# Performance work log

Measured on AMD Instinct MI355X. Metric: run time of the kernel, lower is better.

The kernel has to match this reference:

```python
import jax, jax.numpy as jnp
import numpy as np

NEG_SLOPE = 0.2


def gat_layer(x, src, dst, W, att_src, att_dst, bias, heads, ch, n):
    # x: [N, Din]; W: [Din, heads*ch]
    xl = (x @ W).reshape(n, heads, ch)                # [N, H, C]
    a_s = jnp.sum(xl * att_src[None], axis=-1)        # [N, H]
    a_d = jnp.sum(xl * att_dst[None], axis=-1)        # [N, H]
    e = jax.nn.leaky_relu(a_s[src] + a_d[dst], NEG_SLOPE)   # [E, H]
    # segment softmax over incoming edges per destination node
    emax = jax.ops.segment_max(e, dst, num_segments=n)      # [N, H]
    ex = jnp.exp(e - emax[dst])
    denom = jax.ops.segment_sum(ex, dst, num_segments=n)
    alpha = ex / denom[dst]                                  # [E, H]
    msg = xl[src] * alpha[:, :, None]                        # [E, H, C]
    out = jax.ops.segment_sum(msg, dst, num_segments=n)      # [N, H, C]
    return out.reshape(n, heads * ch) + bias


def setup_inputs() -> dict:
    key = jax.random.key(0)
    ks = jax.random.split(key, 10)
    N, D, H, C, E, NCLS = 10000, 128, 4, 256, 160000, 10
    s = 0.05
    return {
        "x": jax.random.normal(ks[0], (N, D), jnp.float32),
        "edge_index": jax.random.randint(ks[1], (2, E), 0, N, jnp.int64),
        "W1": jax.random.normal(ks[2], (D, H * C), jnp.float32) * s,
        "att_src1": jax.random.normal(ks[3], (H, C), jnp.float32) * s,
        "att_dst1": jax.random.normal(ks[4], (H, C), jnp.float32) * s,
        "b1": jnp.zeros((H * C,), jnp.float32),
        "W2": jax.random.normal(ks[5], (H * C, C), jnp.float32) * s,
        "att_src2": jax.random.normal(ks[6], (1, C), jnp.float32) * s,
        "att_dst2": jax.random.normal(ks[7], (1, C), jnp.float32) * s,
        "b2": jnp.zeros((C,), jnp.float32),
        "Wc": jax.random.normal(ks[8], (C, NCLS), jnp.float32) * s,
        "bc": jnp.zeros((NCLS,), jnp.float32),
    }


def reference(x, edge_index, W1, att_src1, att_dst1, b1, W2, att_src2, att_dst2, b2, Wc, bc):
    n = x.shape[0]
    # PyG GATConv adds self-loops by default
    loops = jnp.arange(n, dtype=edge_index.dtype)
    src = jnp.concatenate([edge_index[0], loops])
    dst = jnp.concatenate([edge_index[1], loops])
    h1 = jax.nn.relu(gat_layer(x, src, dst, W1, att_src1, att_dst1, b1, 4, 256, n))
    h2 = jax.nn.relu(gat_layer(h1, src, dst, W2, att_src2, att_dst2, b2, 1, 256, n))
    z = jnp.mean(h2, axis=0, keepdims=True)[None]   # global_mean_pool (single graph), unsqueeze(0) -> [1,1,C]
    return z @ Wc + bc                               # [1,1,n_cls]
```

## Files before the change

### kernel.cpp

```cpp
#include <hip/hip_runtime.h>
#include <hip/hip_bf16.h>
#include <math.h>

#define NEG_SLOPE 0.2f

typedef __attribute__((ext_vector_type(8))) short short8;
typedef __attribute__((ext_vector_type(4))) float f32x4;

typedef __attribute__((address_space(1))) const void g_void;
typedef __attribute__((address_space(3))) void l_void;

__device__ __forceinline__ float lrelu(float x) { return x > 0.f ? x : NEG_SLOPE * x; }
__device__ __forceinline__ float bf2f(unsigned short u) { return __uint_as_float((unsigned)u << 16); }
__device__ __forceinline__ unsigned short f2bf(float f) {
    unsigned u = __float_as_uint(f);
    unsigned rounding = 0x7fff + ((u >> 16) & 1);
    return (unsigned short)((u + rounding) >> 16);
}

__device__ __forceinline__ void transpose_part(const float* __restrict__ in,
                                               unsigned short* __restrict__ out,
                                               int R, int Cc, int bx, int by,
                                               int tx, int ty)
{
    __shared__ float tile[32][33];
    int c0 = bx * 32, r0 = by * 32;
#pragma unroll
    for (int j = 0; j < 4; ++j)
        tile[ty + j * 8][tx] = in[(size_t)(r0 + ty + j * 8) * Cc + c0 + tx];
    __syncthreads();
#pragma unroll
    for (int j = 0; j < 4; ++j)
        out[(size_t)(c0 + ty + j * 8) * R + r0 + tx] = f2bf(tile[tx][ty + j * 8]);
}

__global__ __launch_bounds__(256) void prep(const float* __restrict__ x,
                                            unsigned short* __restrict__ x_bf,
                                            const float* __restrict__ W1,
                                            unsigned short* __restrict__ w1t,
                                            const float* __restrict__ W2,
                                            unsigned short* __restrict__ w2t,
                                            int n_valid4, int nb_conv)
{
    const int bid = blockIdx.x;
    const int tid = threadIdx.x;
    if (bid < nb_conv) {
        int g = bid * 256 + tid;
        ushort4 o;
        if (g < n_valid4) {
            float4 v = *reinterpret_cast<const float4*>(x + (size_t)g * 4);
            o = make_ushort4(f2bf(v.x), f2bf(v.y), f2bf(v.z), f2bf(v.w));
        } else {
            o = make_ushort4(0, 0, 0, 0);
        }
        *reinterpret_cast<ushort4*>(x_bf + (size_t)g * 4) = o;
    } else if (bid < nb_conv + 128) {
        int b = bid - nb_conv;
        transpose_part(W1, w1t, 128, 1024, b & 31, b >> 5, tid & 31, tid >> 5);
    } else {
        int b = bid - nb_conv - 128;
        transpose_part(W2, w2t, 1024, 256, b & 7, b >> 3, tid & 31, tid >> 5);
    }
}

__global__ __launch_bounds__(256) void watt_k(const unsigned short* __restrict__ w1t,
                                              const float* __restrict__ as1,
                                              const float* __restrict__ ad1,
                                              float* __restrict__ watt)
{
    const int b = blockIdx.x;
    const int h = b >> 1, sd = b & 1;
    const float* att = (sd ? ad1 : as1) + h * 256;
    const int k = threadIdx.x & 127;
    const int chalf = threadIdx.x >> 7;
    float s = 0.f;
#pragma unroll 8
    for (int c = chalf * 128; c < chalf * 128 + 128; ++c)
        s = fmaf(bf2f(w1t[(size_t)(h * 256 + c) * 128 + k]), att[c], s);
    __shared__ float sh[256];
    sh[threadIdx.x] = s;
    __syncthreads();
    if (chalf == 0) watt[sd * 512 + h * 128 + k] = s + sh[128 + k];
}

__global__ __launch_bounds__(256) void score1(const unsigned short* __restrict__ x_bf,
                                              const float* __restrict__ watt,
                                              float* __restrict__ a_s,
                                              float* __restrict__ a_d, int N)
{
    const int n = blockIdx.x * 4 + (threadIdx.x >> 6);
    const int lane = threadIdx.x & 63;
    if (n >= N) return;
    unsigned u = *reinterpret_cast<const unsigned*>(x_bf + (size_t)n * 128 + lane * 2);
    float x0 = bf2f((unsigned short)(u & 0xffff)), x1 = bf2f((unsigned short)(u >> 16));
    float s[4], d[4];
#pragma unroll
    for (int h = 0; h < 4; ++h) {
        float2 ws = *reinterpret_cast<const float2*>(watt + h * 128 + lane * 2);
        float2 wd = *reinterpret_cast<const float2*>(watt + 512 + h * 128 + lane * 2);
        s[h] = x0 * ws.x + x1 * ws.y;
        d[h] = x0 * wd.x + x1 * wd.y;
    }
#pragma unroll
    for (int o = 32; o > 0; o >>= 1) {
#pragma unroll
        for (int h = 0; h < 4; ++h) {
            s[h] += __shfl_xor(s[h], o);
            d[h] += __shfl_xor(d[h], o);
        }
    }
    if (lane == 0) {
        *reinterpret_cast<float4*>(a_s + (size_t)n * 4) = make_float4(s[0], s[1], s[2], s[3]);
        *reinterpret_cast<float4*>(a_d + (size_t)n * 4) = make_float4(d[0], d[1], d[2], d[3]);
    }
}

__global__ __launch_bounds__(256) void gemm_bf16(const unsigned short* __restrict__ A, int lda,
                                                 size_t strideAz,
                                                 const unsigned short* __restrict__ Bt, int ldb,
                                                 size_t strideBz,
                                                 unsigned short* __restrict__ C, int ldc, int colz,
                                                 const float* __restrict__ bias, int relu,
                                                 int K)
{
    __shared__ unsigned short sA[128 * 64];
    __shared__ unsigned short sB[128 * 64];
    const int zb = blockIdx.z;
    A += (size_t)zb * strideAz;
    Bt += (size_t)zb * strideBz;
    const int ccol0 = zb * colz;
    const int tid = threadIdx.x;
    const int lane = tid & 63;
    const int w = tid >> 6;
    const int wr = w >> 1, wc = w & 1;
    const int m0 = blockIdx.y * 128;
    const int n0 = blockIdx.x * 128;

    f32x4 acc[4][4];
#pragma unroll
    for (int i = 0; i < 4; ++i)
#pragma unroll
        for (int j = 0; j < 4; ++j) acc[i][j] = (f32x4){0.f, 0.f, 0.f, 0.f};

    const int lrow = lane >> 3;
    const int lchunk = (lane & 7) ^ lrow;

    for (int k0 = 0; k0 < K; k0 += 64) {
#pragma unroll
        for (int i = 0; i < 4; ++i) {
            int r0 = (w * 4 + i) * 8;
            const unsigned short* g = A + (size_t)(m0 + r0 + lrow) * lda + k0 + lchunk * 8;
            __builtin_amdgcn_global_load_lds((g_void*)g, (l_void*)((char*)sA + r0 * 128), 16, 0, 0);
        }
#pragma unroll
        for (int i = 0; i < 4; ++i) {
            int r0 = (w * 4 + i) * 8;
            const unsigned short* g = Bt + (size_t)(n0 + r0 + lrow) * ldb + k0 + lchunk * 8;
            __builtin_amdgcn_global_load_lds((g_void*)g, (l_void*)((char*)sB + r0 * 128), 16, 0, 0);
        }
        __syncthreads();
#pragma unroll
        for (int kk = 0; kk < 2; ++kk) {
            short8 a[4], b[4];
#pragma unroll
            for (int i = 0; i < 4; ++i) {
                int r = wr * 64 + i * 16 + (lane & 15);
                int sw = (kk * 4 + (lane >> 4)) ^ (r & 7);
                a[i] = *reinterpret_cast<const short8*>(&sA[r * 64 + sw * 8]);
            }
#pragma unroll
            for (int j = 0; j < 4; ++j) {
                int r = wc * 64 + j * 16 + (lane & 15);
                int sw = (kk * 4 + (lane >> 4)) ^ (r & 7);
                b[j] = *reinterpret_cast<const short8*>(&sB[r * 64 + sw * 8]);
            }
#pragma unroll
            for (int i = 0; i < 4; ++i)
#pragma unroll
                for (int j = 0; j < 4; ++j)
                    acc[i][j] = __builtin_amdgcn_mfma_f32_16x16x32_bf16(a[i], b[j], acc[i][j], 0, 0, 0);
        }
        __syncthreads();
    }

#pragma unroll
    for (int i = 0; i < 4; ++i) {
        int row_b = m0 + wr * 64 + i * 16 + (lane >> 4) * 4;
#pragma unroll
        for (int j = 0; j < 4; ++j) {
            int col = n0 + wc * 64 + j * 16 + (lane & 15);
            float bv = bias ? bias[ccol0 + col] : 0.f;
#pragma unroll
            for (int r = 0; r < 4; ++r) {
                float v = acc[i][j][r] + bv;
                if (relu) v = fmaxf(v, 0.f);
                C[(size_t)(row_b + r) * ldc + ccol0 + col] = f2bf(v);
            }
        }
    }
}

__global__ __launch_bounds__(256) void attn_scores(const unsigned short* __restrict__ xl,
                                                   const float* __restrict__ att_s,
                                                   const float* __restrict__ att_d,
                                                   float* __restrict__ a_s,
                                                   float* __restrict__ a_d,
                                                   int NH, int H)
{
    int wid = (blockIdx.x * 256 + threadIdx.x) >> 6;
    int lane = threadIdx.x & 63;
    if (wid >= NH) return;
    int h = wid % H;
    ushort4 v = *reinterpret_cast<const ushort4*>(xl + (size_t)wid * 256 + lane * 4);
    float4 vs = *reinterpret_cast<const float4*>(att_s + h * 256 + lane * 4);
    float4 vd = *reinterpret_cast<const float4*>(att_d + h * 256 + lane * 4);
    float x0 = bf2f(v.x), x1 = bf2f(v.y), x2 = bf2f(v.z), x3 = bf2f(v.w);
    float ss = x0 * vs.x + x1 * vs.y + x2 * vs.z + x3 * vs.w;
    float sd = x0 * vd.x + x1 * vd.y + x2 * vd.z + x3 * vd.w;
#pragma unroll
    for (int o = 32; o > 0; o >>= 1) {
        ss += __shfl_down(ss, o);
        sd += __shfl_down(sd, o);
    }
    if (lane == 0) { a_s[wid] = ss; a_d[wid] = sd; }
}

__global__ __launch_bounds__(256) void count_deg(const int* __restrict__ ei, int E, int E2,
                                                 int* __restrict__ counts)
{
    int e = blockIdx.x * 256 + threadIdx.x;
    if (e >= E2) return;
    int dd = (e < E) ? ei[E + e] : (e - E);
    atomicAdd(&counts[dd], 1);
}

__global__ __launch_bounds__(256) void scan1(const int* __restrict__ counts,
                                             int* __restrict__ offs,
                                             int* __restrict__ btot, int n)
{
    int b = blockIdx.x, tid = threadIdx.x, i = b * 256 + tid;
    int lane = tid & 63, w = tid >> 6;
    int v = (i < n) ? counts[i] : 0;
    int s = v;
#pragma unroll
    for (int o = 1; o < 64; o <<= 1) {
        int t = __shfl_up(s, o);
        if (lane >= o) s += t;
    }
    __shared__ int wsum[4];
    if (lane == 63) wsum[w] = s;
    __syncthreads();
    int base = 0;
#pragma unroll
    for (int k = 0; k < 4; ++k)
        if (k < w) base += wsum[k];
    int incl = s + base;
    if (i < n) offs[i] = incl - v;
    if (tid == 255) btot[b] = incl;
}

__global__ __launch_bounds__(256) void scan2(int* __restrict__ offs,
                                             const int* __restrict__ btot, int n)
{
    int b = blockIdx.x, tid = threadIdx.x, i = b * 256 + tid;
    __shared__ int sbase;
    if (tid < 64) {
        int v = (tid < b) ? btot[tid] : 0;
#pragma unroll
        for (int o = 32; o > 0; o >>= 1) v += __shfl_down(v, o);
        if (tid == 0) sbase = v;
    }
    __syncthreads();
    if (i < n) offs[i] += sbase;
    if (b == (int)gridDim.x - 1 && tid == 255) offs[n] = sbase + btot[b];
}

__global__ __launch_bounds__(256) void scatter_csr(const int* __restrict__ ei, int E, int E2,
                                                   const int* __restrict__ offsets,
                                                   int* __restrict__ cursor,
                                                   int* __restrict__ csr_src)
{
    int e = blockIdx.x * 256 + threadIdx.x;
    if (e >= E2) return;
    int s, dd;
    if (e < E) { s = ei[e]; dd = ei[E + e]; }
    else       { s = e - E; dd = e - E; }
    int pos = offsets[dd] + atomicAdd(&cursor[dd], 1);
    csr_src[pos] = s;
}

__global__ __launch_bounds__(64) void alpha_h4(const float* __restrict__ a_s,
                                               const float* __restrict__ a_d,
                                               const int* __restrict__ offsets,
                                               const int* __restrict__ csr_src,
                                               float* __restrict__ alpha)
{
    const int dst = blockIdx.x;
    const int lane = threadIdx.x;
    const int o0 = offsets[dst];
    const int deg = offsets[dst + 1] - o0;
    const int h = lane & 3;
    const int i0 = lane >> 2;
    const float adh = a_d[dst * 4 + h];

    float m = -1e30f;
    for (int i = i0; i < deg; i += 16)
        m = fmaxf(m, lrelu(a_s[csr_src[o0 + i] * 4 + h] + adh));
#pragma unroll
    for (int o = 4; o < 64; o <<= 1) m = fmaxf(m, __shfl_xor(m, o));
    float sum = 0.f;
    for (int i = i0; i < deg; i += 16)
        sum += __expf(lrelu(a_s[csr_src[o0 + i] * 4 + h] + adh) - m);
#pragma unroll
    for (int o = 4; o < 64; o <<= 1) sum += __shfl_xor(sum, o);
    const float inv = 1.f / sum;
    for (int i = i0; i < deg; i += 16)
        alpha[(size_t)(o0 + i) * 4 + h] =
            __expf(lrelu(a_s[csr_src[o0 + i] * 4 + h] + adh) - m) * inv;
}

__global__ __launch_bounds__(64) void alpha_h1(const float* __restrict__ a_s,
                                               const float* __restrict__ a_d,
                                               const int* __restrict__ offsets,
                                               const int* __restrict__ csr_src,
                                               float* __restrict__ alpha)
{
    const int dst = blockIdx.x;
    const int lane = threadIdx.x;
    const int o0 = offsets[dst];
    const int deg = offsets[dst + 1] - o0;
    const float ad = a_d[dst];

    float m = -1e30f;
    for (int i = lane; i < deg; i += 64)
        m = fmaxf(m, lrelu(a_s[csr_src[o0 + i]] + ad));
#pragma unroll
    for (int o = 1; o < 64; o <<= 1) m = fmaxf(m, __shfl_xor(m, o));
    float sum = 0.f;
    for (int i = lane; i < deg; i += 64)
        sum += __expf(lrelu(a_s[csr_src[o0 + i]] + ad) - m);
#pragma unroll
    for (int o = 1; o < 64; o <<= 1) sum += __shfl_xor(sum, o);
    const float inv = 1.f / sum;
    for (int i = lane; i < deg; i += 64)
        alpha[o0 + i] = __expf(lrelu(a_s[csr_src[o0 + i]] + ad) - m) * inv;
}

__global__ __launch_bounds__(256) void zgather(const unsigned short* __restrict__ x_bf,
                                               const float* __restrict__ alpha,
                                               const int* __restrict__ offs,
                                               const int* __restrict__ csr,
                                               unsigned short* __restrict__ z,
                                               int N, int Mpad)
{
    const int wid = threadIdx.x >> 6, lane = threadIdx.x & 63;
    const int dst = blockIdx.x * 4 + wid;
    if (dst >= Mpad) return;
    const size_t zoff = (size_t)dst * 128 + lane * 2;
    if (dst >= N) {
#pragma unroll
        for (int h = 0; h < 4; ++h)
            *reinterpret_cast<unsigned*>(z + (size_t)h * Mpad * 128 + zoff) = 0u;
        return;
    }
    const int o0 = offs[dst];
    const int deg = offs[dst + 1] - o0;

    float acc[8];
#pragma unroll
    for (int k = 0; k < 8; ++k) acc[k] = 0.f;

    int i = 0;
    for (; i + 1 < deg; i += 2) {
        int e0 = o0 + i, e1 = e0 + 1;
        int s0 = csr[e0], s1 = csr[e1];
        float4 a0 = *reinterpret_cast<const float4*>(alpha + (size_t)e0 * 4);
        float4 a1 = *reinterpret_cast<const float4*>(alpha + (size_t)e1 * 4);
        unsigned u0 = *reinterpret_cast<const unsigned*>(x_bf + (size_t)s0 * 128 + lane * 2);
        unsigned u1 = *reinterpret_cast<const unsigned*>(x_bf + (size_t)s1 * 128 + lane * 2);
        float x00 = bf2f((unsigned short)(u0 & 0xffff)), x01 = bf2f((unsigned short)(u0 >> 16));
        float x10 = bf2f((unsigned short)(u1 & 0xffff)), x11 = bf2f((unsigned short)(u1 >> 16));
        acc[0] = fmaf(a0.x, x00, acc[0]); acc[1] = fmaf(a0.x, x01, acc[1]);
        acc[2] = fmaf(a0.y, x00, acc[2]); acc[3] = fmaf(a0.y, x01, acc[3]);
        acc[4] = fmaf(a0.z, x00, acc[4]); acc[5] = fmaf(a0.z, x01, acc[5]);
        acc[6] = fmaf(a0.w, x00, acc[6]); acc[7] = fmaf(a0.w, x01, acc[7]);
        acc[0] = fmaf(a1.x, x10, acc[0]); acc[1] = fmaf(a1.x, x11, acc[1]);
        acc[2] = fmaf(a1.y, x10, acc[2]); acc[3] = fmaf(a1.y, x11, acc[3]);
        acc[4] = fmaf(a1.z, x10, acc[4]); acc[5] = fmaf(a1.z, x11, acc[5]);
        acc[6] = fmaf(a1.w, x10, acc[6]); acc[7] = fmaf(a1.w, x11, acc[7]);
    }
    if (i < deg) {
        int e0 = o0 + i;
        int s0 = csr[e0];
        float4 a0 = *reinterpret_cast<const float4*>(alpha + (size_t)e0 * 4);
        unsigned u0 = *reinterpret_cast<const unsigned*>(x_bf + (size_t)s0 * 128 + lane * 2);
        float x00 = bf2f((unsigned short)(u0 & 0xffff)), x01 = bf2f((unsigned short)(u0 >> 16));
        acc[0] = fmaf(a0.x, x00, acc[0]); acc[1] = fmaf(a0.x, x01, acc[1]);
        acc[2] = fmaf(a0.y, x00, acc[2]); acc[3] = fmaf(a0.y, x01, acc[3]);
        acc[4] = fmaf(a0.z, x00, acc[4]); acc[5] = fmaf(a0.z, x01, acc[5]);
        acc[6] = fmaf(a0.w, x00, acc[6]); acc[7] = fmaf(a0.w, x01, acc[7]);
    }
#pragma unroll
    for (int h = 0; h < 4; ++h) {
        unsigned o = (unsigned)f2bf(acc[h * 2]) | ((unsigned)f2bf(acc[h * 2 + 1]) << 16);
        *reinterpret_cast<unsigned*>(z + (size_t)h * Mpad * 128 + zoff) = o;
    }
}

template <int PLOG>
__global__ __launch_bounds__(256) void gather2(const unsigned short* __restrict__ xl,
                                               const float* __restrict__ alpha,
                                               const int* __restrict__ offsets,
                                               const int* __restrict__ csr_src,
                                               const float* __restrict__ bias,
                                               float* __restrict__ outb, int N)
{
    const int panel = blockIdx.x & ((1 << PLOG) - 1);
    const int dstq = blockIdx.x >> PLOG;
    const int wid = threadIdx.x >> 6;
    const int lane = threadIdx.x & 63;
    const int dst = dstq * 4 + wid;
    if (dst >= N) return;
    const int g = lane >> 4;
    const int cb = panel * 128 + (lane & 15) * 8;

    const int o0 = offsets[dst];
    const int deg = offsets[dst + 1] - o0;

    float acc[8];
#pragma unroll
    for (int k = 0; k < 8; ++k) acc[k] = 0.f;

    int i = g;
    for (; i + 4 < deg; i += 8) {
        int e0 = o0 + i, e1 = e0 + 4;
        int s0 = csr_src[e0], s1 = csr_src[e1];
        float al0 = alpha[e0], al1 = alpha[e1];
        short8 v0 = *reinterpret_cast<const short8*>(xl + (size_t)s0 * 256 + cb);
        short8 v1 = *reinterpret_cast<const short8*>(xl + (size_t)s1 * 256 + cb);
#pragma unroll
        for (int k = 0; k < 8; ++k) {
            acc[k] = fmaf(al0, bf2f((unsigned short)v0[k]), acc[k]);
            acc[k] = fmaf(al1, bf2f((unsigned short)v1[k]), acc[k]);
        }
    }
    for (; i < deg; i += 4) {
        int e = o0 + i;
        int s = csr_src[e];
        float al = alpha[e];
        short8 v = *reinterpret_cast<const short8*>(xl + (size_t)s * 256 + cb);
#pragma unroll
        for (int k = 0; k < 8; ++k)
            acc[k] = fmaf(al, bf2f((unsigned short)v[k]), acc[k]);
    }
#pragma unroll
    for (int k = 0; k < 8; ++k) {
        acc[k] += __shfl_xor(acc[k], 16);
        acc[k] += __shfl_xor(acc[k], 32);
    }

    if (lane < 16) {
        float4 b0 = *reinterpret_cast<const float4*>(bias + cb);
        float4 b1 = *reinterpret_cast<const float4*>(bias + cb + 4);
        float4 r0, r1;
        r0.x = fmaxf(acc[0] + b0.x, 0.f); r0.y = fmaxf(acc[1] + b0.y, 0.f);
        r0.z = fmaxf(acc[2] + b0.z, 0.f); r0.w = fmaxf(acc[3] + b0.w, 0.f);
        r1.x = fmaxf(acc[4] + b1.x, 0.f); r1.y = fmaxf(acc[5] + b1.y, 0.f);
        r1.z = fmaxf(acc[6] + b1.z, 0.f); r1.w = fmaxf(acc[7] + b1.w, 0.f);
        *reinterpret_cast<float4*>(outb + (size_t)dst * 256 + cb) = r0;
        *reinterpret_cast<float4*>(outb + (size_t)dst * 256 + cb + 4) = r1;
    }
}

__global__ __launch_bounds__(256) void mean_pool(const float* __restrict__ h2,
                                                 float* __restrict__ meanv, int N)
{
    int c = threadIdx.x;
    float s = 0.f;
    for (int r = blockIdx.x; r < N; r += gridDim.x)
        s += h2[(size_t)r * 256 + c];
    atomicAdd(&meanv[c], s);
}

__global__ __launch_bounds__(64) void final_k(const float* __restrict__ meanv,
                                              const float* __restrict__ Wc,
                                              const float* __restrict__ bc,
                                              float* __restrict__ out, int N, int NCLS)
{
    int k = threadIdx.x;
    if (k >= NCLS) return;
    float invN = 1.f / (float)N;
    float s = 0.f;
    for (int c = 0; c < 256; ++c)
        s = fmaf(meanv[c] * invN, Wc[c * NCLS + k], s);
    out[k] = s + bc[k];
}

extern "C" void kernel_launch(void* const* d_in, const int* in_sizes, int n_in,
                              void* d_out, int out_size, void* d_ws, size_t ws_size,
                              hipStream_t stream)
{
    const float* x   = (const float*)d_in[0];
    const int*   ei  = (const int*)d_in[1];
    const float* W1  = (const float*)d_in[2];
    const float* as1 = (const float*)d_in[3];
    const float* ad1 = (const float*)d_in[4];
    const float* b1  = (const float*)d_in[5];
    const float* W2  = (const float*)d_in[6];
    const float* as2 = (const float*)d_in[7];
    const float* ad2 = (const float*)d_in[8];
    const float* b2  = (const float*)d_in[9];
    const float* Wc  = (const float*)d_in[10];
    const float* bc  = (const float*)d_in[11];
    float* out = (float*)d_out;

    const int D = 128, H = 4, C = 256, HC = 1024;
    const int N = in_sizes[0] / D;
    const int E = in_sizes[1] / 2;
    const int E2 = E + N;
    const int NCLS = in_sizes[11];
    const int Mpad = ((N + 127) / 128) * 128;
    const int NB = (N + 255) / 256;
    const int NB_CONV = Mpad * D / 4 / 256;

    char* ws = (char*)d_ws;
    size_t woff = 0;
    auto take = [&](size_t bytes) -> char* {
        char* p = ws + woff;
        woff += (bytes + 255) & ~(size_t)255;
        return p;
    };
    unsigned short* x_bf  = (unsigned short*)take((size_t)Mpad * D * 2);
    unsigned short* w1t   = (unsigned short*)take((size_t)HC * D * 2);
    unsigned short* w2t   = (unsigned short*)take((size_t)C * HC * 2);
    unsigned short* z     = (unsigned short*)take((size_t)4 * Mpad * 128 * 2);
    unsigned short* h1    = (unsigned short*)take((size_t)Mpad * HC * 2);
    unsigned short* xl2   = (unsigned short*)take((size_t)Mpad * C * 2);
    float* h2     = (float*)take((size_t)N * C * 4);
    float* watt   = (float*)take(1024 * 4);
    float* a_s1   = (float*)take((size_t)N * H * 4);
    float* a_d1   = (float*)take((size_t)N * H * 4);
    float* a_s2   = (float*)take((size_t)N * 4);
    float* a_d2   = (float*)take((size_t)N * 4);
    float* alpha1 = (float*)take((size_t)E2 * H * 4);
    float* alpha2 = (float*)take((size_t)E2 * 4);
    int*   offs   = (int*)take((size_t)(N + 1) * 4);
    int*   btot   = (int*)take(64 * 4);
    int*   csrsrc = (int*)take((size_t)E2 * 4);
    char* zero_base = ws + woff;
    int*   counts = (int*)take((size_t)N * 4);
    int*   cursor = (int*)take((size_t)N * 4);
    float* meanv  = (float*)take(256 * 4);
    size_t zero_bytes = (size_t)((ws + woff) - zero_base);

    hipMemsetAsync(zero_base, 0, zero_bytes, stream);

    prep<<<NB_CONV + 128 + 256, 256, 0, stream>>>(x, x_bf, W1, w1t, W2, w2t,
                                                  N * D / 4, NB_CONV);

    count_deg<<<(E2 + 255) / 256, 256, 0, stream>>>(ei, E, E2, counts);
    scan1<<<NB, 256, 0, stream>>>(counts, offs, btot, N);
    scan2<<<NB, 256, 0, stream>>>(offs, btot, N);
    scatter_csr<<<(E2 + 255) / 256, 256, 0, stream>>>(ei, E, E2, offs, cursor, csrsrc);

    watt_k<<<8, 256, 0, stream>>>(w1t, as1, ad1, watt);
    score1<<<(N + 3) / 4, 256, 0, stream>>>(x_bf, watt, a_s1, a_d1, N);
    alpha_h4<<<N, 64, 0, stream>>>(a_s1, a_d1, offs, csrsrc, alpha1);
    zgather<<<(Mpad + 3) / 4, 256, 0, stream>>>(x_bf, alpha1, offs, csrsrc, z, N, Mpad);
    gemm_bf16<<<dim3(2, Mpad / 128, 4), 256, 0, stream>>>(
        z, 128, (size_t)Mpad * 128, w1t, 128, (size_t)256 * 128,
        h1, 1024, 256, b1, 1, 128);

    gemm_bf16<<<dim3(2, Mpad / 128, 1), 256, 0, stream>>>(
        h1, 1024, 0, w2t, 1024, 0, xl2, 256, 0, nullptr, 0, 1024);
    attn_scores<<<(N + 3) / 4, 256, 0, stream>>>(xl2, as2, ad2, a_s2, a_d2, N, 1);
    alpha_h1<<<N, 64, 0, stream>>>(a_s2, a_d2, offs, csrsrc, alpha2);
    gather2<1><<<((N + 3) / 4) * 2, 256, 0, stream>>>(xl2, alpha2, offs, csrsrc, b2, h2, N);

    mean_pool<<<640, 256, 0, stream>>>(h2, meanv, N);
    final_k<<<1, 64, 0, stream>>>(meanv, Wc, bc, out, N, NCLS);
}
```

Before: 241.4 us.

## Fuse edge softmax into gather kernels and add narrow-tile GEMM for layer two

Removes the separate alpha kernels for both layers. The gather kernels now compute the unnormalized exp(leaky_relu) weights on the fly, accumulate the normalizer alongside the weighted features, and divide at the end. This drops the alpha buffers and two launches. It also dispatches the layer-2 projection (N=256 output columns) to a new 128x64-tile MFMA GEMM to get more blocks in flight. Skipping the max subtraction risks overflow for large attention logits, though the logits here are small.

```diff
diff --git a/kernel.cpp b/kernel.cpp
--- a/kernel.cpp
+++ b/kernel.cpp
@@ -200,6 +200,79 @@
     }
 }
 
+__global__ __launch_bounds__(256) void gemm_n64(const unsigned short* __restrict__ A, int lda,
+                                                const unsigned short* __restrict__ Bt, int ldb,
+                                                unsigned short* __restrict__ C, int ldc,
+                                                int K)
+{
+    __shared__ unsigned short sA[128 * 64];
+    __shared__ unsigned short sB[64 * 64];
+    const int tid = threadIdx.x;
+    const int lane = tid & 63;
+    const int w = tid >> 6;
+    const int m0 = blockIdx.y * 128;
+    const int n0 = blockIdx.x * 64;
+
+    f32x4 acc[2][4];
+#pragma unroll
+    for (int i = 0; i < 2; ++i)
+#pragma unroll
+        for (int j = 0; j < 4; ++j) acc[i][j] = (f32x4){0.f, 0.f, 0.f, 0.f};
+
+    const int lrow = lane >> 3;
+    const int lchunk = (lane & 7) ^ lrow;
+
+    for (int k0 = 0; k0 < K; k0 += 64) {
+#pragma unroll
+        for (int i = 0; i < 4; ++i) {
+            int r0 = (w * 4 + i) * 8;
+            const unsigned short* g = A + (size_t)(m0 + r0 + lrow) * lda + k0 + lchunk * 8;
+            __builtin_amdgcn_global_load_lds((g_void*)g, (l_void*)((char*)sA + r0 * 128), 16, 0, 0);
+        }
+#pragma unroll
+        for (int i = 0; i < 2; ++i) {
+            int r0 = (w * 2 + i) * 8;
+            const unsigned short* g = Bt + (size_t)(n0 + r0 + lrow) * ldb + k0 + lchunk * 8;
+            __builtin_amdgcn_global_load_lds((g_void*)g, (l_void*)((char*)sB + r0 * 128), 16, 0, 0);
+        }
+        __syncthreads();
+#pragma unroll
+        for (int kk = 0; kk < 2; ++kk) {
+            short8 a[2], b[4];
+#pragma unroll
+            for (int i = 0; i < 2; ++i) {
+                int r = w * 32 + i * 16 + (lane & 15);
+                int sw = (kk * 4 + (lane >> 4)) ^ (r & 7);
+                a[i] = *reinterpret_cast<const short8*>(&sA[r * 64 + sw * 8]);
+            }
+#pragma unroll
+            for (int j = 0; j < 4; ++j) {
+                int r = j * 16 + (lane & 15);
+                int sw = (kk * 4 + (lane >> 4)) ^ (r & 7);
+                b[j] = *reinterpret_cast<const short8*>(&sB[r * 64 + sw * 8]);
+            }
+#pragma unroll
+            for (int i = 0; i < 2; ++i)
+#pragma unroll
+                for (int j = 0; j < 4; ++j)
+                    acc[i][j] = __builtin_amdgcn_mfma_f32_16x16x32_bf16(a[i], b[j], acc[i][j], 0, 0, 0);
+        }
+        __syncthreads();
+    }
+
+#pragma unroll
+    for (int i = 0; i < 2; ++i) {
+        int row_b = m0 + w * 32 + i * 16 + (lane >> 4) * 4;
+#pragma unroll
+        for (int j = 0; j < 4; ++j) {
+            int col = n0 + j * 16 + (lane & 15);
+#pragma unroll
+            for (int r = 0; r < 4; ++r)
+                C[(size_t)(row_b + r) * ldc + col] = f2bf(acc[i][j][r]);
+        }
+    }
+}
+
 __global__ __launch_bounds__(256) void attn_scores(const unsigned short* __restrict__ xl,
                                                    const float* __restrict__ att_s,
                                                    const float* __restrict__ att_d,
@@ -289,69 +362,13 @@
     csr_src[pos] = s;
 }
 
-__global__ __launch_bounds__(64) void alpha_h4(const float* __restrict__ a_s,
-                                               const float* __restrict__ a_d,
-                                               const int* __restrict__ offsets,
-                                               const int* __restrict__ csr_src,
-                                               float* __restrict__ alpha)
-{
-    const int dst = blockIdx.x;
-    const int lane = threadIdx.x;
-    const int o0 = offsets[dst];
-    const int deg = offsets[dst + 1] - o0;
-    const int h = lane & 3;
-    const int i0 = lane >> 2;
-    const float adh = a_d[dst * 4 + h];
-
-    float m = -1e30f;
-    for (int i = i0; i < deg; i += 16)
-        m = fmaxf(m, lrelu(a_s[csr_src[o0 + i] * 4 + h] + adh));
-#pragma unroll
-    for (int o = 4; o < 64; o <<= 1) m = fmaxf(m, __shfl_xor(m, o));
-    float sum = 0.f;
-    for (int i = i0; i < deg; i += 16)
-        sum += __expf(lrelu(a_s[csr_src[o0 + i] * 4 + h] + adh) - m);
-#pragma unroll
-    for (int o = 4; o < 64; o <<= 1) sum += __shfl_xor(sum, o);
-    const float inv = 1.f / sum;
-    for (int i = i0; i < deg; i += 16)
-        alpha[(size_t)(o0 + i) * 4 + h] =
-            __expf(lrelu(a_s[csr_src[o0 + i] * 4 + h] + adh) - m) * inv;
-}
-
-__global__ __launch_bounds__(64) void alpha_h1(const float* __restrict__ a_s,
-                                               const float* __restrict__ a_d,
-                                               const int* __restrict__ offsets,
-                                               const int* __restrict__ csr_src,
-                                               float* __restrict__ alpha)
-{
-    const int dst = blockIdx.x;
-    const int lane = threadIdx.x;
-    const int o0 = offsets[dst];
-    const int deg = offsets[dst + 1] - o0;
-    const float ad = a_d[dst];
-
-    float m = -1e30f;
-    for (int i = lane; i < deg; i += 64)
-        m = fmaxf(m, lrelu(a_s[csr_src[o0 + i]] + ad));
-#pragma unroll
-    for (int o = 1; o < 64; o <<= 1) m = fmaxf(m, __shfl_xor(m, o));
-    float sum = 0.f;
-    for (int i = lane; i < deg; i += 64)
-        sum += __expf(lrelu(a_s[csr_src[o0 + i]] + ad) - m);
-#pragma unroll
-    for (int o = 1; o < 64; o <<= 1) sum += __shfl_xor(sum, o);
-    const float inv = 1.f / sum;
-    for (int i = lane; i < deg; i += 64)
-        alpha[o0 + i] = __expf(lrelu(a_s[csr_src[o0 + i]] + ad) - m) * inv;
-}
-
-__global__ __launch_bounds__(256) void zgather(const unsigned short* __restrict__ x_bf,
-                                               const float* __restrict__ alpha,
-                                               const int* __restrict__ offs,
-                                               const int* __restrict__ csr,
-                                               unsigned short* __restrict__ z,
-                                               int N, int Mpad)
+__global__ __launch_bounds__(256) void zgather_f(const unsigned short* __restrict__ x_bf,
+                                                 const float* __restrict__ a_s1,
+                                                 const float* __restrict__ a_d1,
+                                                 const int* __restrict__ offs,
+                                                 const int* __restrict__ csr,
+                                                 unsigned short* __restrict__ z,
+                                                 int N, int Mpad)
 {
     const int wid = threadIdx.x >> 6, lane = threadIdx.x & 63;
     const int dst = blockIdx.x * 4 + wid;
@@ -365,64 +382,77 @@
     }
     const int o0 = offs[dst];
     const int deg = offs[dst + 1] - o0;
+    const float4 ad = *reinterpret_cast<const float4*>(a_d1 + (size_t)dst * 4);
 
     float acc[8];
 #pragma unroll
     for (int k = 0; k < 8; ++k) acc[k] = 0.f;
+    float sm0 = 0.f, sm1 = 0.f, sm2 = 0.f, sm3 = 0.f;
 
     int i = 0;
     for (; i + 1 < deg; i += 2) {
         int e0 = o0 + i, e1 = e0 + 1;
         int s0 = csr[e0], s1 = csr[e1];
-        float4 a0 = *reinterpret_cast<const float4*>(alpha + (size_t)e0 * 4);
-        float4 a1 = *reinterpret_cast<const float4*>(alpha + (size_t)e1 * 4);
+        float4 as0 = *reinterpret_cast<const float4*>(a_s1 + (size_t)s0 * 4);
+        float4 as1 = *reinterpret_cast<const float4*>(a_s1 + (size_t)s1 * 4);
         unsigned u0 = *reinterpret_cast<const unsigned*>(x_bf + (size_t)s0 * 128 + lane * 2);
         unsigned u1 = *reinterpret_cast<const unsigned*>(x_bf + (size_t)s1 * 128 + lane * 2);
+        float w00 = __expf(lrelu(as0.x + ad.x)), w01 = __expf(lrelu(as0.y + ad.y));
+        float w02 = __expf(lrelu(as0.z + ad.z)), w03 = __expf(lrelu(as0.w + ad.w));
+        float w10 = __expf(lrelu(as1.x + ad.x)), w11 = __expf(lrelu(as1.y + ad.y));
+        float w12 = __expf(lrelu(as1.z + ad.z)), w13 = __expf(lrelu(as1.w + ad.w));
+        sm0 += w00 + w10; sm1 += w01 + w11; sm2 += w02 + w12; sm3 += w03 + w13;
         float x00 = bf2f((unsigned short)(u0 & 0xffff)), x01 = bf2f((unsigned short)(u0 >> 16));
         float x10 = bf2f((unsigned short)(u1 & 0xffff)), x11 = bf2f((unsigned short)(u1 >> 16));
-        acc[0] = fmaf(a0.x, x00, acc[0]); acc[1] = fmaf(a0.x, x01, acc[1]);
-        acc[2] = fmaf(a0.y, x00, acc[2]); acc[3] = fmaf(a0.y, x01, acc[3]);
-        acc[4] = fmaf(a0.z, x00, acc[4]); acc[5] = fmaf(a0.z, x01, acc[5]);
-        acc[6] = fmaf(a0.w, x00, acc[6]); acc[7] = fmaf(a0.w, x01, acc[7]);
-        acc[0] = fmaf(a1.x, x10, acc[0]); acc[1] = fmaf(a1.x, x11, acc[1]);
-        acc[2] = fmaf(a1.y, x10, acc[2]); acc[3] = fmaf(a1.y, x11, acc[3]);
-        acc[4] = fmaf(a1.z, x10, acc[4]); acc[5] = fmaf(a1.z, x11, acc[5]);
-        acc[6] = fmaf(a1.w, x10, acc[6]); acc[7] = fmaf(a1.w, x11, acc[7]);
+        acc[0] = fmaf(w00, x00, acc[0]); acc[1] = fmaf(w00, x01, acc[1]);
+        acc[2] = fmaf(w01, x00, acc[2]); acc[3] = fmaf(w01, x01, acc[3]);
+        acc[4] = fmaf(w02, x00, acc[4]); acc[5] = fmaf(w02, x01, acc[5]);
+        acc[6] = fmaf(w03, x00, acc[6]); acc[7] = fmaf(w03, x01, acc[7]);
+        acc[0] = fmaf(w10, x10, acc[0]); acc[1] = fmaf(w10, x11, acc[1]);
+        acc[2] = fmaf(w11, x10, acc[2]); acc[3] = fmaf(w11, x11, acc[3]);
+        acc[4] = fmaf(w12, x10, acc[4]); acc[5] = fmaf(w12, x11, acc[5]);
+        acc[6] = fmaf(w13, x10, acc[6]); acc[7] = fmaf(w13, x11, acc[7]);
     }
     if (i < deg) {
         int e0 = o0 + i;
         int s0 = csr[e0];
-        float4 a0 = *reinterpret_cast<const float4*>(alpha + (size_t)e0 * 4);
+        float4 as0 = *reinterpret_cast<const float4*>(a_s1 + (size_t)s0 * 4);
         unsigned u0 = *reinterpret_cast<const unsigned*>(x_bf + (size_t)s0 * 128 + lane * 2);
+        float w00 = __expf(lrelu(as0.x + ad.x)), w01 = __expf(lrelu(as0.y + ad.y));
+        float w02 = __expf(lrelu(as0.z + ad.z)), w03 = __expf(lrelu(as0.w + ad.w));
+        sm0 += w00; sm1 += w01; sm2 += w02; sm3 += w03;
         float x00 = bf2f((unsigned short)(u0 & 0xffff)), x01 = bf2f((unsigned short)(u0 >> 16));
-        acc[0] = fmaf(a0.x, x00, acc[0]); acc[1] = fmaf(a0.x, x01, acc[1]);
-        acc[2] = fmaf(a0.y, x00, acc[2]); acc[3] = fmaf(a0.y, x01, acc[3]);
-        acc[4] = fmaf(a0.z, x00, acc[4]); acc[5] = fmaf(a0.z, x01, acc[5]);
-        acc[6] = fmaf(a0.w, x00, acc[6]); acc[7] = fmaf(a0.w, x01, acc[7]);
-    }
+        acc[0] = fmaf(w00, x00, acc[0]); acc[1] = fmaf(w00, x01, acc[1]);
+        acc[2] = fmaf(w01, x00, acc[2]); acc[3] = fmaf(w01, x01, acc[3]);
+        acc[4] = fmaf(w02, x00, acc[4]); acc[5] = fmaf(w02, x01, acc[5]);
+        acc[6] = fmaf(w03, x00, acc[6]); acc[7] = fmaf(w03, x01, acc[7]);
+    }
+    float inv[4] = {1.f / sm0, 1.f / sm1, 1.f / sm2, 1.f / sm3};
 #pragma unroll
     for (int h = 0; h < 4; ++h) {
-        unsigned o = (unsigned)f2bf(acc[h * 2]) | ((unsigned)f2bf(acc[h * 2 + 1]) << 16);
+        unsigned o = (unsigned)f2bf(acc[h * 2] * inv[h]) |
+                     ((unsigned)f2bf(acc[h * 2 + 1] * inv[h]) << 16);
         *reinterpret_cast<unsigned*>(z + (size_t)h * Mpad * 128 + zoff) = o;
     }
 }
 
-template <int PLOG>
-__global__ __launch_bounds__(256) void gather2(const unsigned short* __restrict__ xl,
-                                               const float* __restrict__ alpha,
-                                               const int* __restrict__ offsets,
-                                               const int* __restrict__ csr_src,
-                                               const float* __restrict__ bias,
-                                               float* __restrict__ outb, int N)
-{
-    const int panel = blockIdx.x & ((1 << PLOG) - 1);
-    const int dstq = blockIdx.x >> PLOG;
+__global__ __launch_bounds__(256) void gather2_f(const unsigned short* __restrict__ xl,
+                                                 const float* __restrict__ a_s,
+                                                 const float* __restrict__ a_d,
+                                                 const int* __restrict__ offsets,
+                                                 const int* __restrict__ csr_src,
+                                                 const float* __restrict__ bias,
+                                                 float* __restrict__ outb, int N)
+{
+    const int panel = blockIdx.x & 1;
+    const int dstq = blockIdx.x >> 1;
     const int wid = threadIdx.x >> 6;
     const int lane = threadIdx.x & 63;
     const int dst = dstq * 4 + wid;
     if (dst >= N) return;
     const int g = lane >> 4;
     const int cb = panel * 128 + (lane & 15) * 8;
+    const float ad = a_d[dst];
 
     const int o0 = offsets[dst];
     const int deg = offsets[dst + 1] - o0;
@@ -430,29 +460,35 @@
     float acc[8];
 #pragma unroll
     for (int k = 0; k < 8; ++k) acc[k] = 0.f;
+    float ssum = 0.f;
 
     int i = g;
     for (; i + 4 < deg; i += 8) {
         int e0 = o0 + i, e1 = e0 + 4;
         int s0 = csr_src[e0], s1 = csr_src[e1];
-        float al0 = alpha[e0], al1 = alpha[e1];
+        float w0 = __expf(lrelu(a_s[s0] + ad));
+        float w1 = __expf(lrelu(a_s[s1] + ad));
+        ssum += w0 + w1;
         short8 v0 = *reinterpret_cast<const short8*>(xl + (size_t)s0 * 256 + cb);
         short8 v1 = *reinterpret_cast<const short8*>(xl + (size_t)s1 * 256 + cb);
 #pragma unroll
         for (int k = 0; k < 8; ++k) {
-            acc[k] = fmaf(al0, bf2f((unsigned short)v0[k]), acc[k]);
-            acc[k] = fmaf(al1, bf2f((unsigned short)v1[k]), acc[k]);
+            acc[k] = fmaf(w0, bf2f((unsigned short)v0[k]), acc[k]);
+            acc[k] = fmaf(w1, bf2f((unsigned short)v1[k]), acc[k]);
         }
     }
     for (; i < deg; i += 4) {
         int e = o0 + i;
         int s = csr_src[e];
-        float al = alpha[e];
+        float w = __expf(lrelu(a_s[s] + ad));
+        ssum += w;
         short8 v = *reinterpret_cast<const short8*>(xl + (size_t)s * 256 + cb);
 #pragma unroll
         for (int k = 0; k < 8; ++k)
-            acc[k] = fmaf(al, bf2f((unsigned short)v[k]), acc[k]);
-    }
+            acc[k] = fmaf(w, bf2f((unsigned short)v[k]), acc[k]);
+    }
+    ssum += __shfl_xor(ssum, 16);
+    ssum += __shfl_xor(ssum, 32);
 #pragma unroll
     for (int k = 0; k < 8; ++k) {
         acc[k] += __shfl_xor(acc[k], 16);
@@ -460,13 +496,14 @@
     }
 
     if (lane < 16) {
+        const float inv = 1.f / ssum;
         float4 b0 = *reinterpret_cast<const float4*>(bias + cb);
         float4 b1 = *reinterpret_cast<const float4*>(bias + cb + 4);
         float4 r0, r1;
-        r0.x = fmaxf(acc[0] + b0.x, 0.f); r0.y = fmaxf(acc[1] + b0.y, 0.f);
-        r0.z = fmaxf(acc[2] + b0.z, 0.f); r0.w = fmaxf(acc[3] + b0.w, 0.f);
-        r1.x = fmaxf(acc[4] + b1.x, 0.f); r1.y = fmaxf(acc[5] + b1.y, 0.f);
-        r1.z = fmaxf(acc[6] + b1.z, 0.f); r1.w = fmaxf(acc[7] + b1.w, 0.f);
+        r0.x = fmaxf(acc[0] * inv + b0.x, 0.f); r0.y = fmaxf(acc[1] * inv + b0.y, 0.f);
+        r0.z = fmaxf(acc[2] * inv + b0.z, 0.f); r0.w = fmaxf(acc[3] * inv + b0.w, 0.f);
+        r1.x = fmaxf(acc[4] * inv + b1.x, 0.f); r1.y = fmaxf(acc[5] * inv + b1.y, 0.f);
+        r1.z = fmaxf(acc[6] * inv + b1.z, 0.f); r1.w = fmaxf(acc[7] * inv + b1.w, 0.f);
         *reinterpret_cast<float4*>(outb + (size_t)dst * 256 + cb) = r0;
         *reinterpret_cast<float4*>(outb + (size_t)dst * 256 + cb + 4) = r1;
     }
@@ -542,8 +579,6 @@
     float* a_d1   = (float*)take((size_t)N * H * 4);
     float* a_s2   = (float*)take((size_t)N * 4);
     float* a_d2   = (float*)take((size_t)N * 4);
-    float* alpha1 = (float*)take((size_t)E2 * H * 4);
-    float* alpha2 = (float*)take((size_t)E2 * 4);
     int*   offs   = (int*)take((size_t)(N + 1) * 4);
     int*   btot   = (int*)take(64 * 4);
     int*   csrsrc = (int*)take((size_t)E2 * 4);
@@ -565,17 +600,15 @@
 
     watt_k<<<8, 256, 0, stream>>>(w1t, as1, ad1, watt);
     score1<<<(N + 3) / 4, 256, 0, stream>>>(x_bf, watt, a_s1, a_d1, N);
-    alpha_h4<<<N, 64, 0, stream>>>(a_s1, a_d1, offs, csrsrc, alpha1);
-    zgather<<<(Mpad + 3) / 4, 256, 0, stream>>>(x_bf, alpha1, offs, csrsrc, z, N, Mpad);
+    zgather_f<<<(Mpad + 3) / 4, 256, 0, stream>>>(x_bf, a_s1, a_d1, offs, csrsrc, z, N, Mpad);
     gemm_bf16<<<dim3(2, Mpad / 128, 4), 256, 0, stream>>>(
         z, 128, (size_t)Mpad * 128, w1t, 128, (size_t)256 * 128,
         h1, 1024, 256, b1, 1, 128);
 
-    gemm_bf16<<<dim3(2, Mpad / 128, 1), 256, 0, stream>>>(
-        h1, 1024, 0, w2t, 1024, 0, xl2, 256, 0, nullptr, 0, 1024);
+    gemm_n64<<<dim3(C / 64, Mpad / 128), 256, 0, stream>>>(
+        h1, 1024, w2t, 1024, xl2, 256, 1024);
     attn_scores<<<(N + 3) / 4, 256, 0, stream>>>(xl2, as2, ad2, a_s2, a_d2, N, 1);
-    alpha_h1<<<N, 64, 0, stream>>>(a_s2, a_d2, offs, csrsrc, alpha2);
-    gather2<1><<<((N + 3) / 4) * 2, 256, 0, stream>>>(xl2, alpha2, offs, csrsrc, b2, h2, N);
+    gather2_f<<<((N + 3) / 4) * 2, 256, 0, stream>>>(xl2, a_s2, a_d2, offs, csrsrc, b2, h2, N);
 
     mean_pool<<<640, 256, 0, stream>>>(h2, meanv, N);
     final_k<<<1, 64, 0, stream>>>(meanv, Wc, bc, out, N, NCLS);
```

Result: faster. 229.7 us (-4.9%).
